# Kernel tuning notes

Measured on AMD Instinct MI355X. Metric: run time of the kernel, lower is better.

Reference implementation:

```python
import jax, jax.numpy as jnp
import numpy as np

B, N0, C, K, D = 16384, 1024, 12, 64, 3  # batch, feat dim, num_classes, num_clusters, ndim


def setup_inputs() -> dict:
    key = jax.random.key(0)
    ks = jax.random.split(key, 6)
    s = 0.02  # weight init scale
    return {
        "x": jax.random.normal(ks[0], (B, N0), dtype=jnp.float32),
        "Wfc": jax.random.normal(ks[1], (N0, C), dtype=jnp.float32) * s,
        "bfc": jnp.zeros((C,), dtype=jnp.float32),
        "Wbin": jax.random.normal(ks[2], (C, K, N0), dtype=jnp.float32) * s,
        "bbin": jnp.zeros((C, K), dtype=jnp.float32),
        "Wres": jax.random.normal(ks[3], (C, K, N0, D), dtype=jnp.float32) * s,
        "bres": jnp.zeros((C, K, D), dtype=jnp.float32),
        "centers": jax.random.normal(ks[4], (K, D), dtype=jnp.float32),
    }


def reference(x, Wfc, bfc, Wbin, bbin, Wres, bres, centers):
    # category head
    y0 = x @ Wfc + bfc                                            # [B, C]
    # per-class bin logits (batched over all classes at once)
    ybin = jnp.einsum("bn,ckn->bck", x, Wbin) + bbin              # [B, C, K]
    ind = jnp.argmax(ybin, axis=2)                                # [B, C] selected cluster per class
    # multires path: all (class, cluster) expert residuals, then one-hot select
    yres_all = jnp.einsum("bn,cknd->bckd", x, Wres) + bres        # [B, C, K, D]
    yres = jnp.take_along_axis(
        yres_all, ind[:, :, None, None], axis=2
    ).squeeze(2)                                                  # [B, C, D]
    # gather cluster centers and add residual
    y = centers[ind] + yres                                       # [B, C, D]
    # torch: stack over classes -> [C,B,D]; permute(1,2,0) -> [B, D, C]
    y1 = jnp.transpose(y, (0, 2, 1))                              # [B, D, C]
    return (y0, y1)
```

## Files before the change

### kernel.cpp

```cpp
#include <hip/hip_runtime.h>

typedef unsigned int uint32;
typedef unsigned long long uint64;
typedef unsigned short ushort16;
typedef __attribute__((ext_vector_type(8))) short bf16x8;
typedef __attribute__((ext_vector_type(4))) float f32x4;
typedef __attribute__((ext_vector_type(4))) uint32 u32x4;

#define B_SZ 16384
#define MARGIN 0.02f

__device__ __forceinline__ ushort16 f2bf(float f) {
  uint32 u = __float_as_uint(f);
  u += 0x7fffu + ((u >> 16) & 1u);
  return (ushort16)(u >> 16);
}
__device__ __forceinline__ float bf2f(ushort16 h) { return __uint_as_float(((uint32)h) << 16); }
__device__ __forceinline__ float bflo(uint32 u) { return __uint_as_float(u << 16); }
__device__ __forceinline__ float bfhi(uint32 u) { return __uint_as_float(u & 0xffff0000u); }
__device__ __forceinline__ uint32 pk2(float lo, float hi) {
  return ((uint32)f2bf(hi) << 16) | (uint32)f2bf(lo);
}
__device__ __forceinline__ int dot4(uint32 a, uint32 b, int c) {
#if __has_builtin(__builtin_amdgcn_sdot4)
  return __builtin_amdgcn_sdot4((int)a, (int)b, c, false);
#else
  int s = c;
#pragma unroll
  for (int k = 0; k < 4; ++k)
    s += (int)(char)(a >> (8 * k)) * (int)(char)(b >> (8 * k));
  return s;
#endif
}
__device__ __forceinline__ int q8(float v, float inv) {
  int q = (int)rintf(v * inv);
  return q > 127 ? 127 : (q < -127 ? -127 : q);
}

__global__ __launch_bounds__(256) void prep_all(
    const float* __restrict__ Wfc, const float* __restrict__ Wbin,
    const float* __restrict__ Wres, const float* __restrict__ x,
    ushort16* __restrict__ Wall, uint32* __restrict__ wq, float* __restrict__ swk,
    uint2* __restrict__ xb, uint32* __restrict__ xq, float* __restrict__ sxb) {
  __shared__ float red[256];
  const int blk = blockIdx.x;
  const int t = threadIdx.x;
  if (blk < 3584) {
    int idx = blk * 256 + t;
    int j = idx >> 10, n = idx & 1023;
    float v = 0.f;
    if (j < 12) v = Wfc[n * 12 + j];
    else if (j >= 64 && j < 832) v = Wbin[(size_t)(j - 64) * 1024 + n];
    Wall[idx] = f2bf(v);
  } else if (blk < 4352) {
    const int ck = blk - 3584;
    const float4* base4 = (const float4*)(Wres + (size_t)ck * 3072);
    float4 v0 = base4[3 * t], v1 = base4[3 * t + 1], v2 = base4[3 * t + 2];
    float vals[12] = {v0.x, v0.y, v0.z, v0.w, v1.x, v1.y, v1.z, v1.w, v2.x, v2.y, v2.z, v2.w};
    float m = 0.f;
#pragma unroll
    for (int i = 0; i < 12; ++i) m = fmaxf(m, fabsf(vals[i]));
    red[t] = m; __syncthreads();
    for (int s = 128; s; s >>= 1) { if (t < s) red[t] = fmaxf(red[t], red[t + s]); __syncthreads(); }
    float mx = fmaxf(red[0], 1e-20f);
    float inv = 127.f / mx;
    if (t == 0) swk[ck] = mx / 127.f;
#pragma unroll
    for (int d = 0; d < 3; ++d) {
      uint32 u = 0;
#pragma unroll
      for (int j = 0; j < 4; ++j)
        u |= ((uint32)(unsigned char)(char)q8(vals[j * 3 + d], inv)) << (8 * j);
      wq[((size_t)(ck * 3 + d) << 8) + t] = u;
    }
  } else {
    const int lane = t & 63;
    const int b = (blk - 4352) * 4 + (t >> 6);
    const float4* xr = (const float4*)(x + (size_t)b * 1024 + lane * 16);
    float4 v0 = xr[0], v1 = xr[1], v2 = xr[2], v3 = xr[3];
    float xv[16] = {v0.x, v0.y, v0.z, v0.w, v1.x, v1.y, v1.z, v1.w,
                    v2.x, v2.y, v2.z, v2.w, v3.x, v3.y, v3.z, v3.w};
    u32x4 pa, pb;
    pa.x = pk2(xv[0], xv[1]);  pa.y = pk2(xv[2], xv[3]);
    pa.z = pk2(xv[4], xv[5]);  pa.w = pk2(xv[6], xv[7]);
    pb.x = pk2(xv[8], xv[9]);  pb.y = pk2(xv[10], xv[11]);
    pb.z = pk2(xv[12], xv[13]); pb.w = pk2(xv[14], xv[15]);
    u32x4* xbrow = (u32x4*)((uint32*)xb + (size_t)b * 512);
    xbrow[2 * lane] = pa;
    xbrow[2 * lane + 1] = pb;
    float m = 0.f;
#pragma unroll
    for (int i = 0; i < 16; ++i) m = fmaxf(m, fabsf(xv[i]));
    for (int off = 32; off; off >>= 1) m = fmaxf(m, __shfl_xor(m, off));
    float mx = fmaxf(m, 1e-20f);
    float inv = 127.f / mx;
    if (lane == 0) sxb[b] = mx / 127.f;
    u32x4 qv;
#pragma unroll
    for (int q = 0; q < 4; ++q) {
      uint32 u = ((uint32)(unsigned char)(char)q8(xv[4 * q + 0], inv)) |
                 ((uint32)(unsigned char)(char)q8(xv[4 * q + 1], inv)) << 8 |
                 ((uint32)(unsigned char)(char)q8(xv[4 * q + 2], inv)) << 16 |
                 ((uint32)(unsigned char)(char)q8(xv[4 * q + 3], inv)) << 24;
      qv[q] = u;
    }
    ((u32x4*)(xq + (size_t)b * 256))[lane] = qv;
  }
}

__global__ void prep_wall_f(const float* __restrict__ Wfc, const float* __restrict__ Wbin,
                            ushort16* __restrict__ Wall) {
  int idx = blockIdx.x * 256 + threadIdx.x;
  int j = idx >> 10, n = idx & 1023;
  float v = 0.f;
  if (j < 12) v = Wfc[n * 12 + j];
  else if (j >= 64 && j < 832) v = Wbin[(size_t)(j - 64) * 1024 + n];
  Wall[idx] = f2bf(v);
}
__global__ void prep_wres(const float* __restrict__ Wres, ushort16* __restrict__ Wres_b) {
  int idx = blockIdx.x * 256 + threadIdx.x;
  int n = idx & 1023;
  int d = (idx >> 10) % 3;
  int ck = idx / 3072;
  Wres_b[idx] = f2bf(Wres[((size_t)ck * 1024 + n) * 3 + d]);
}

template<int XB>
__global__ __launch_bounds__(256) void gemm_mfma(
    const float* __restrict__ x, const ushort16* __restrict__ xb,
    const float* __restrict__ bfc, const float* __restrict__ bbin,
    const ushort16* __restrict__ Wall, ushort16* __restrict__ ybin,
    unsigned char* __restrict__ ind8, uint64* __restrict__ mask64,
    float* __restrict__ out) {
  __shared__ __align__(16) char smem[65536];
  const int t = threadIdx.x;
  const int lane = t & 63, wid = t >> 6;
  const int wm = wid & 1, wn = wid >> 1;

  int orig = blockIdx.x;
  int bid = (orig & 7) * 112 + (orig >> 3);
  int nb = bid % 7, mb = bid / 7;
  const int b0 = mb * 128;

  f32x4 acc[4][4];
#pragma unroll
  for (int i = 0; i < 4; ++i)
#pragma unroll
    for (int j = 0; j < 4; ++j) acc[i][j] = (f32x4){0.f, 0.f, 0.f, 0.f};

  const int lr = lane & 15, lq = lane >> 4;
  const int fxor = (lr & 7) << 4;
  const int gs = (lane & 7) ^ (lane >> 3);
  const int grw = lane >> 3;

#define GLDS(srcp, dstoff)                                                      \
  __builtin_amdgcn_global_load_lds(                                             \
      (const __attribute__((address_space(1))) uint32*)(srcp),                  \
      (__attribute__((address_space(3))) uint32*)(smem + (dstoff)), 16, 0, 0)

  if (XB) {
#pragma unroll
    for (int i = 0; i < 4; ++i) {
      int ch = i * 4 + wid, row = ch * 8 + grw;
      GLDS(xb + (size_t)(b0 + row) * 1024 + gs * 8, ch * 1024);
      GLDS(Wall + (size_t)(nb * 128 + row) * 1024 + gs * 8, 16384 + ch * 1024);
    }
    asm volatile("s_waitcnt vmcnt(0)" ::: "memory");
    __builtin_amdgcn_s_barrier();
    int cur = 0;
#pragma unroll 1
    for (int tt = 0; tt < 16; ++tt) {
      if (tt < 15) {
        int kc = (tt + 1) * 64;
        int nbase = (cur ^ 1) * 32768;
#pragma unroll
        for (int i = 0; i < 4; ++i) {
          int ch = i * 4 + wid, row = ch * 8 + grw;
          GLDS(xb + (size_t)(b0 + row) * 1024 + kc + gs * 8, nbase + ch * 1024);
          GLDS(Wall + (size_t)(nb * 128 + row) * 1024 + kc + gs * 8, nbase + 16384 + ch * 1024);
        }
      }
      asm volatile("" ::: "memory");
      const char* base = smem + cur * 32768;
#pragma unroll
      for (int kk = 0; kk < 2; ++kk) {
        int cbx = (kk * 64 + lq * 16) ^ fxor;
        bf16x8 af[4], bfr[4];
#pragma unroll
        for (int i = 0; i < 4; ++i)
          af[i] = *(const bf16x8*)(base + (wm * 64 + i * 16 + lr) * 128 + cbx);
#pragma unroll
        for (int j = 0; j < 4; ++j)
          bfr[j] = *(const bf16x8*)(base + 16384 + (wn * 64 + j * 16 + lr) * 128 + cbx);
#pragma unroll
        for (int i = 0; i < 4; ++i)
#pragma unroll
          for (int j = 0; j < 4; ++j)
            acc[i][j] = __builtin_amdgcn_mfma_f32_16x16x32_bf16(af[i], bfr[j], acc[i][j], 0, 0, 0);
      }
      if (tt < 15) {
        asm volatile("s_waitcnt vmcnt(0)" ::: "memory");
        __builtin_amdgcn_s_barrier();
        cur ^= 1;
      }
    }
  } else {
    for (int kc = 0; kc < 1024; kc += 64) {
      __syncthreads();
      const int sxor = ((t >> 3) & 7) << 4;
#pragma unroll
      for (int i = 0; i < 4; ++i) {
        int s = t + i * 256;
        int row = s >> 3, c8 = (s & 7) * 8;
        int dst = row * 128 + ((c8 * 2) ^ sxor);
        const float4* src = (const float4*)(x + (size_t)(b0 + row) * 1024 + kc + c8);
        float4 v0 = src[0], v1 = src[1];
        u32x4 pv;
        pv.x = pk2(v0.x, v0.y); pv.y = pk2(v0.z, v0.w);
        pv.z = pk2(v1.x, v1.y); pv.w = pk2(v1.z, v1.w);
        *(u32x4*)(smem + dst) = pv;
      }
#pragma unroll
      for (int i = 0; i < 4; ++i) {
        int s = t + i * 256;
        int row = s >> 3, c8 = (s & 7) * 8;
        int dst = 16384 + row * 128 + ((c8 * 2) ^ sxor);
        u32x4 v = *(const u32x4*)(Wall + (size_t)(nb * 128 + row) * 1024 + kc + c8);
        *(u32x4*)(smem + dst) = v;
      }
      __syncthreads();
#pragma unroll
      for (int kk = 0; kk < 2; ++kk) {
        int cbx = (kk * 64 + lq * 16) ^ fxor;
        bf16x8 af[4], bfr[4];
#pragma unroll
        for (int i = 0; i < 4; ++i)
          af[i] = *(const bf16x8*)(smem + (wm * 64 + i * 16 + lr) * 128 + cbx);
#pragma unroll
        for (int j = 0; j < 4; ++j)
          bfr[j] = *(const bf16x8*)(smem + 16384 + (wn * 64 + j * 16 + lr) * 128 + cbx);
#pragma unroll
        for (int i = 0; i < 4; ++i)
#pragma unroll
          for (int j = 0; j < 4; ++j)
            acc[i][j] = __builtin_amdgcn_mfma_f32_16x16x32_bf16(af[i], bfr[j], acc[i][j], 0, 0, 0);
      }
    }
  }
#undef GLDS

  const int g = 2 * nb + wn;
  if (g == 0) {
#pragma unroll
    for (int i = 0; i < 4; ++i)
#pragma unroll
      for (int r = 0; r < 4; ++r) {
        int gm = b0 + wm * 64 + i * 16 + lq * 4 + r;
        if (lr < 12) out[(size_t)gm * 12 + lr] = acc[i][0][r] + bfc[lr];
      }
    return;
  }
  if (g > 12) return;
  const int c = g - 1;
  if (XB == 0) {
#pragma unroll
    for (int i = 0; i < 4; ++i)
#pragma unroll
      for (int j = 0; j < 4; ++j)
#pragma unroll
        for (int r = 0; r < 4; ++r) {
          int gm = b0 + wm * 64 + i * 16 + lq * 4 + r;
          int col = j * 16 + lr;
          ybin[((size_t)gm * 12 + c) * 64 + col] = f2bf(acc[i][j][r] + bbin[c * 64 + col]);
        }
    return;
  }
  float bb[4];
#pragma unroll
  for (int j = 0; j < 4; ++j) bb[j] = bbin[c * 64 + j * 16 + lr];
#pragma unroll
  for (int i = 0; i < 4; ++i)
#pragma unroll
    for (int r = 0; r < 4; ++r) {
      float v0 = acc[i][0][r] + bb[0], v1 = acc[i][1][r] + bb[1];
      float v2 = acc[i][2][r] + bb[2], v3 = acc[i][3][r] + bb[3];
      float m1 = v0, m2 = -3.4e38f; int k1 = lr;
      if (v1 > m1) { m2 = m1; m1 = v1; k1 = 16 + lr; } else m2 = fmaxf(m2, v1);
      if (v2 > m1) { m2 = m1; m1 = v2; k1 = 32 + lr; } else m2 = fmaxf(m2, v2);
      if (v3 > m1) { m2 = m1; m1 = v3; k1 = 48 + lr; } else m2 = fmaxf(m2, v3);
#pragma unroll
      for (int off = 1; off < 16; off <<= 1) {
        float om1 = __shfl_xor(m1, off);
        int   ok1 = __shfl_xor(k1, off);
        float om2 = __shfl_xor(m2, off);
        bool take = (om1 > m1) || (om1 == m1 && ok1 < k1);
        float lose = take ? m1 : om1;
        m2 = fmaxf(fmaxf(m2, om2), lose);
        if (take) { m1 = om1; k1 = ok1; }
      }
      float thr = m1 - MARGIN;
      uint64 bl0 = __ballot(v0 >= thr);
      uint64 bl1 = __ballot(v1 >= thr);
      uint64 bl2 = __ballot(v2 >= thr);
      uint64 bl3 = __ballot(v3 >= thr);
      if (lr == 0) {
        int row = wm * 64 + i * 16 + lq * 4 + r;
        uint64 mk = ((bl0 >> (lq * 16)) & 0xffffull) |
                    (((bl1 >> (lq * 16)) & 0xffffull) << 16) |
                    (((bl2 >> (lq * 16)) & 0xffffull) << 32) |
                    (((bl3 >> (lq * 16)) & 0xffffull) << 48);
        int gp = (b0 + row) * 12 + c;
        ind8[gp] = (unsigned char)(k1 | ((m1 - m2 <= MARGIN) ? 128 : 0));
        mask64[gp] = mk;
      }
    }
}

__global__ __launch_bounds__(256) void compact_k(const unsigned char* __restrict__ ind8,
                                                 uint32* __restrict__ cnt,
                                                 uint32* __restrict__ wl) {
  const int b = blockIdx.x * 256 + threadIdx.x;
  const int lane = threadIdx.x & 63;
  const uint32* p = (const uint32*)(ind8 + b * 12);
  uint32 d0 = p[0], d1 = p[1], d2 = p[2];
  uint32 fmask = 0;
#pragma unroll
  for (int j = 0; j < 4; ++j) {
    if ((d0 >> (8 * j)) & 128u) fmask |= 1u << j;
    if ((d1 >> (8 * j)) & 128u) fmask |= 1u << (4 + j);
    if ((d2 >> (8 * j)) & 128u) fmask |= 1u << (8 + j);
  }
  uint64 bal = __ballot(fmask != 0);
  uint32 base = 0;
  if (lane == 0 && bal) base = atomicAdd(cnt, (uint32)__popcll(bal));
  base = __shfl(base, 0);
  if (fmask) {
    int rank = (int)__popcll(bal & ((1ull << lane) - 1ull));
    wl[base + rank] = (uint32)b | (fmask << 14);
  }
}

__global__ __launch_bounds__(256) void tail_k(
    const float* __restrict__ x, const float* __restrict__ Wbin,
    const float* __restrict__ bbin, const float* __restrict__ bres,
    const float* __restrict__ centers, const unsigned char* __restrict__ ind8,
    const uint64* __restrict__ mask64, const uint32* __restrict__ wq,
    const float* __restrict__ swk, const uint32* __restrict__ xq,
    const float* __restrict__ sxb, const uint32* __restrict__ cnt,
    const uint32* __restrict__ wl, float* __restrict__ out) {
  const int lane = threadIdx.x & 63;
  const int w = threadIdx.x >> 6;

  if (blockIdx.x < 4096) {
    const uint32 wv_id = blockIdx.x * 4 + w;
    if (wv_id >= *cnt) return;
    const uint32 e = wl[wv_id];
    const int b = (int)(e & 16383u);
    uint32 fmask = e >> 14;

    float xv[16];
    const float4* xr = (const float4*)(x + (size_t)b * 1024 + lane * 16);
#pragma unroll
    for (int q = 0; q < 4; ++q) {
      float4 vv = xr[q];
      xv[4 * q] = vv.x; xv[4 * q + 1] = vv.y; xv[4 * q + 2] = vv.z; xv[4 * q + 3] = vv.w;
    }
    const float sx = sxb[b];
    const float inv = (sx > 0.f) ? 1.f / sx : 0.f;
    uint32 xi[4];
#pragma unroll
    for (int q = 0; q < 4; ++q)
      xi[q] = ((uint32)(unsigned char)(char)q8(xv[4 * q + 0], inv)) |
              ((uint32)(unsigned char)(char)q8(xv[4 * q + 1], inv)) << 8 |
              ((uint32)(unsigned char)(char)q8(xv[4 * q + 2], inv)) << 16 |
              ((uint32)(unsigned char)(char)q8(xv[4 * q + 3], inv)) << 24;
    const size_t obase = (size_t)B_SZ * 12 + (size_t)b * 36;

#pragma unroll 1
    while (fmask) {
      const int c = __ffs(fmask) - 1;
      fmask &= fmask - 1;
      uint64 mask = mask64[b * 12 + c];
      double best = -1.0e300;
      int bk = 0;
#pragma unroll 1
      while (mask) {
        int kk[4];
        int nc = 0;
        while (mask && nc < 4) { kk[nc++] = __ffsll(mask) - 1; mask &= mask - 1; }
#pragma unroll
        for (int j = 1; j < 4; ++j) if (j >= nc) kk[j] = kk[0];
        double s[4] = {0.0, 0.0, 0.0, 0.0};
#pragma unroll
        for (int ci = 0; ci < 4; ++ci) {
          const float4* wr4 = (const float4*)(Wbin + ((size_t)c * 64 + kk[ci]) * 1024 + lane * 16);
#pragma unroll
          for (int q = 0; q < 4; ++q) {
            float4 wvv = wr4[q];
            s[ci] += (double)xv[4 * q] * (double)wvv.x + (double)xv[4 * q + 1] * (double)wvv.y +
                     (double)xv[4 * q + 2] * (double)wvv.z + (double)xv[4 * q + 3] * (double)wvv.w;
          }
        }
        for (int off = 32; off; off >>= 1) {
#pragma unroll
          for (int ci = 0; ci < 4; ++ci) s[ci] += __shfl_xor(s[ci], off);
        }
#pragma unroll
        for (int ci = 0; ci < 4; ++ci) {
          double sv = s[ci] + (double)bbin[c * 64 + kk[ci]];
          if (ci < nc && sv > best) { best = sv; bk = kk[ci]; }
        }
      }
      const int ck = c * 64 + bk;
      const uint32* wr = wq + (size_t)ck * 768;
      int acc[3];
#pragma unroll
      for (int d = 0; d < 3; ++d) {
        u32x4 wvq = *(const u32x4*)(wr + d * 256 + lane * 4);
        int ss = dot4(xi[0], wvq.x, 0);
        ss = dot4(xi[1], wvq.y, ss);
        ss = dot4(xi[2], wvq.z, ss);
        acc[d] = dot4(xi[3], wvq.w, ss);
      }
      for (int off = 32; off; off >>= 1) {
        acc[0] += __shfl_xor(acc[0], off);
        acc[1] += __shfl_xor(acc[1], off);
        acc[2] += __shfl_xor(acc[2], off);
      }
      if (lane == 0) {
        float sc = sx * swk[ck];
        out[obase + 0 * 12 + c] = centers[bk * 3 + 0] + bres[ck * 3 + 0] + sc * (float)acc[0];
        out[obase + 1 * 12 + c] = centers[bk * 3 + 1] + bres[ck * 3 + 1] + sc * (float)acc[1];
        out[obase + 2 * 12 + c] = centers[bk * 3 + 2] + bres[ck * 3 + 2] + sc * (float)acc[2];
      }
    }
    return;
  }

  const int b = blockIdx.x - 4096;

  const u32x4 xi = *(const u32x4*)(xq + (size_t)b * 256 + lane * 4);
  const float sx = sxb[b];
  const size_t obase = (size_t)B_SZ * 12 + (size_t)b * 36;

  int iv[3], ind[3], ck[3];
  u32x4 wv[3][3];
#pragma unroll
  for (int cc = 0; cc < 3; ++cc) {
    int c = w * 3 + cc;
    iv[cc] = ind8[b * 12 + c];
    ind[cc] = iv[cc] & 63;
    ck[cc] = c * 64 + ind[cc];
    const uint32* wr = wq + (size_t)ck[cc] * 768;
#pragma unroll
    for (int d = 0; d < 3; ++d)
      wv[cc][d] = *(const u32x4*)(wr + d * 256 + lane * 4);
  }
  int acc[3][3];
#pragma unroll
  for (int cc = 0; cc < 3; ++cc)
#pragma unroll
    for (int d = 0; d < 3; ++d) {
      int s = dot4(xi.x, wv[cc][d].x, 0);
      s = dot4(xi.y, wv[cc][d].y, s);
      s = dot4(xi.z, wv[cc][d].z, s);
      acc[cc][d] = dot4(xi.w, wv[cc][d].w, s);
    }
  for (int off = 32; off; off >>= 1) {
#pragma unroll
    for (int cc = 0; cc < 3; ++cc)
#pragma unroll
      for (int d = 0; d < 3; ++d)
        acc[cc][d] += __shfl_xor(acc[cc][d], off);
  }
  if (lane == 0) {
#pragma unroll
    for (int cc = 0; cc < 3; ++cc) {
      if (iv[cc] & 128) continue;
      int c = w * 3 + cc;
      float sc = sx * swk[ck[cc]];
      out[obase + 0 * 12 + c] = centers[ind[cc] * 3 + 0] + bres[ck[cc] * 3 + 0] + sc * (float)acc[cc][0];
      out[obase + 1 * 12 + c] = centers[ind[cc] * 3 + 1] + bres[ck[cc] * 3 + 1] + sc * (float)acc[cc][1];
      out[obase + 2 * 12 + c] = centers[ind[cc] * 3 + 2] + bres[ck[cc] * 3 + 2] + sc * (float)acc[cc][2];
    }
  }
}

__global__ __launch_bounds__(256) void select2(
    const float* __restrict__ x, const float* __restrict__ Wbin,
    const float* __restrict__ bbin, const float* __restrict__ bres,
    const float* __restrict__ centers, const ushort16* __restrict__ Wres_b,
    const ushort16* __restrict__ ybin, float* __restrict__ out) {
  const int lane = threadIdx.x & 63;
  const int w = threadIdx.x >> 6;
  const int b = blockIdx.x;
  float xv[16];
  {
    const float4* xr = (const float4*)(x + (size_t)b * 1024 + lane * 16);
#pragma unroll
    for (int q = 0; q < 4; ++q) {
      float4 v = xr[q];
      xv[4 * q] = v.x; xv[4 * q + 1] = v.y; xv[4 * q + 2] = v.z; xv[4 * q + 3] = v.w;
    }
  }
  const size_t obase = (size_t)B_SZ * 12 + (size_t)b * 36;
#pragma unroll 1
  for (int cc = 0; cc < 3; ++cc) {
    const int c = w * 3 + cc;
    float v = bf2f(ybin[((size_t)b * 12 + c) * 64 + lane]);
    float m1 = v, m2 = -3.4e38f;
    int k1 = lane;
    for (int off = 32; off; off >>= 1) {
      float om1 = __shfl_xor(m1, off);
      int   ok1 = __shfl_xor(k1, off);
      float om2 = __shfl_xor(m2, off);
      bool take = (om1 > m1) || (om1 == m1 && ok1 < k1);
      float lose = take ? m1 : om1;
      m2 = fmaxf(fmaxf(m2, om2), lose);
      if (take) { m1 = om1; k1 = ok1; }
    }
    int ind = k1;
    if (m1 - m2 <= MARGIN) {
      unsigned long long mask = __ballot(v >= m1 - MARGIN);
      double best = -1.0e300;
      int bk = 0;
      while (mask) {
        int k = __ffsll(mask) - 1;
        mask &= (mask - 1);
        const float4* wr4 = (const float4*)(Wbin + ((size_t)c * 64 + k) * 1024 + lane * 16);
        double s = 0.0;
#pragma unroll
        for (int q = 0; q < 4; ++q) {
          float4 wv = wr4[q];
          s += (double)xv[4 * q] * (double)wv.x + (double)xv[4 * q + 1] * (double)wv.y +
               (double)xv[4 * q + 2] * (double)wv.z + (double)xv[4 * q + 3] * (double)wv.w;
        }
        for (int off = 32; off; off >>= 1) s += __shfl_xor(s, off);
        s += (double)bbin[c * 64 + k];
        if (s > best) { best = s; bk = k; }
      }
      ind = bk;
    }
    const ushort16* wr = Wres_b + ((size_t)(c * 64 + ind) * 3) * 1024;
    float a[3] = {0.f, 0.f, 0.f};
#pragma unroll
    for (int d = 0; d < 3; ++d) {
      const u32x4* pp = (const u32x4*)(wr + d * 1024 + lane * 16);
      u32x4 w0 = pp[0], w1 = pp[1];
      uint32 uw[8] = {w0.x, w0.y, w0.z, w0.w, w1.x, w1.y, w1.z, w1.w};
#pragma unroll
      for (int q = 0; q < 8; ++q) {
        a[d] = fmaf(xv[2 * q],     bflo(uw[q]), a[d]);
        a[d] = fmaf(xv[2 * q + 1], bfhi(uw[q]), a[d]);
      }
    }
    for (int off = 32; off; off >>= 1) {
      a[0] += __shfl_xor(a[0], off);
      a[1] += __shfl_xor(a[1], off);
      a[2] += __shfl_xor(a[2], off);
    }
    if (lane == 0) {
      int ck = c * 64 + ind;
      out[obase + 0 * 12 + c] = centers[ind * 3 + 0] + bres[ck * 3 + 0] + a[0];
      out[obase + 1 * 12 + c] = centers[ind * 3 + 1] + bres[ck * 3 + 1] + a[1];
      out[obase + 2 * 12 + c] = centers[ind * 3 + 2] + bres[ck * 3 + 2] + a[2];
    }
  }
}

extern "C" void kernel_launch(void* const* d_in, const int* in_sizes, int n_in,
                              void* d_out, int out_size, void* d_ws, size_t ws_size,
                              hipStream_t stream) {
  const float* x       = (const float*)d_in[0];
  const float* Wfc     = (const float*)d_in[1];
  const float* bfc     = (const float*)d_in[2];
  const float* Wbin    = (const float*)d_in[3];
  const float* bbin    = (const float*)d_in[4];
  const float* Wres    = (const float*)d_in[5];
  const float* bres    = (const float*)d_in[6];
  const float* centers = (const float*)d_in[7];
  float* out = (float*)d_out;

  char* ws = (char*)d_ws;
  ushort16* Wall = (ushort16*)ws;
  if (ws_size >= 56430592ull) {
    uint32*        wq     = (uint32*)(ws + 1835008);
    float*         swk    = (float*)(ws + 4194304);
    unsigned char* ind8   = (unsigned char*)(ws + 4197376);
    uint64*        mask64 = (uint64*)(ws + 4393984);
    ushort16*      xb     = (ushort16*)(ws + 5966848);
    uint32*        xq     = (uint32*)(ws + 39521280);
    float*         sxb    = (float*)(ws + 56298496);
    uint32*        cnt    = (uint32*)(ws + 56364032);
    uint32*        wl     = (uint32*)(ws + 56364288);

    hipMemsetAsync(cnt, 0, 4, stream);
    prep_all<<<8448, 256, 0, stream>>>(Wfc, Wbin, Wres, x, Wall, wq, swk,
                                       (uint2*)xb, xq, sxb);
    gemm_mfma<1><<<896, 256, 0, stream>>>(x, xb, bfc, bbin, Wall,
                                          (ushort16*)nullptr, ind8, mask64, out);
    compact_k<<<64, 256, 0, stream>>>(ind8, cnt, wl);
    tail_k<<<20480, 256, 0, stream>>>(x, Wbin, bbin, bres, centers, ind8, mask64,
                                      wq, swk, xq, sxb, cnt, wl, out);
  } else {
    ushort16* Wres_b = (ushort16*)(ws + 1835008);
    ushort16* ybin   = (ushort16*)(ws + 6553600);
    prep_wall_f<<<3584, 256, 0, stream>>>(Wfc, Wbin, Wall);
    prep_wres<<<9216, 256, 0, stream>>>(Wres, Wres_b);
    gemm_mfma<0><<<896, 256, 0, stream>>>(x, (const ushort16*)ws, bfc, bbin, Wall,
                                          ybin, (unsigned char*)nullptr,
                                          (uint64*)nullptr, out);
    select2<<<B_SZ, 256, 0, stream>>>(x, Wbin, bbin, bres, centers, Wres_b, ybin, out);
  }
}
```

Before: 159.5 us.

## Deepen GEMM LDS pipeline to four-stage ring of half-K tiles

Replaces the double-buffered 64-wide K tiles in the bf16 MFMA path with a 4-slot ring of 32-wide K tiles, keeping three stages of async global-to-LDS loads in flight and using partial vmcnt waits. The aim is to hide global load latency better and avoid draining all outstanding loads each iteration. In exchange it needs twice as many barriers per K, a changed swizzle for 64-byte rows, and more careful vmcnt accounting. A read of a ring slot that a later stage overwrites would be a correctness risk.

```diff
diff --git a/kernel.cpp b/kernel.cpp
--- a/kernel.cpp
+++ b/kernel.cpp
@@ -149,9 +149,6 @@
     for (int j = 0; j < 4; ++j) acc[i][j] = (f32x4){0.f, 0.f, 0.f, 0.f};
 
   const int lr = lane & 15, lq = lane >> 4;
-  const int fxor = (lr & 7) << 4;
-  const int gs = (lane & 7) ^ (lane >> 3);
-  const int grw = lane >> 3;
 
 #define GLDS(srcp, dstoff)                                                      \
   __builtin_amdgcn_global_load_lds(                                             \
@@ -159,52 +156,52 @@
       (__attribute__((address_space(3))) uint32*)(smem + (dstoff)), 16, 0, 0)
 
   if (XB) {
-#pragma unroll
-    for (int i = 0; i < 4; ++i) {
-      int ch = i * 4 + wid, row = ch * 8 + grw;
-      GLDS(xb + (size_t)(b0 + row) * 1024 + gs * 8, ch * 1024);
-      GLDS(Wall + (size_t)(nb * 128 + row) * 1024 + gs * 8, 16384 + ch * 1024);
-    }
-    asm volatile("s_waitcnt vmcnt(0)" ::: "memory");
-    __builtin_amdgcn_s_barrier();
-    int cur = 0;
+    const int gs2 = (lane & 3) ^ ((lane >> 2) & 3);
+    const int grw2 = lane >> 2;
+    const int ch0 = wid * 2, ch1 = wid * 2 + 1;
+    const ushort16* arow0 = xb + (size_t)(b0 + ch0 * 16 + grw2) * 1024 + gs2 * 8;
+    const ushort16* arow1 = xb + (size_t)(b0 + ch1 * 16 + grw2) * 1024 + gs2 * 8;
+    const ushort16* brow0 = Wall + (size_t)(nb * 128 + ch0 * 16 + grw2) * 1024 + gs2 * 8;
+    const ushort16* brow1 = Wall + (size_t)(nb * 128 + ch1 * 16 + grw2) * 1024 + gs2 * 8;
+
+#define STAGE_HALF(h)                                                           \
+    {                                                                           \
+      int bb_ = ((h) & 3) * 16384;                                              \
+      int kc_ = (h) * 32;                                                       \
+      GLDS(arow0 + kc_, bb_ + ch0 * 1024);                                      \
+      GLDS(arow1 + kc_, bb_ + ch1 * 1024);                                      \
+      GLDS(brow0 + kc_, bb_ + 8192 + ch0 * 1024);                               \
+      GLDS(brow1 + kc_, bb_ + 8192 + ch1 * 1024);                               \
+    }
+
+    STAGE_HALF(0); STAGE_HALF(1); STAGE_HALF(2);
+    const int cbx2 = (lq * 16) ^ ((lr & 3) << 4);
+    const int arow_off = (wm * 64 + lr) * 64;
+    const int brow_off = (wn * 64 + lr) * 64;
 #pragma unroll 1
-    for (int tt = 0; tt < 16; ++tt) {
-      if (tt < 15) {
-        int kc = (tt + 1) * 64;
-        int nbase = (cur ^ 1) * 32768;
-#pragma unroll
-        for (int i = 0; i < 4; ++i) {
-          int ch = i * 4 + wid, row = ch * 8 + grw;
-          GLDS(xb + (size_t)(b0 + row) * 1024 + kc + gs * 8, nbase + ch * 1024);
-          GLDS(Wall + (size_t)(nb * 128 + row) * 1024 + kc + gs * 8, nbase + 16384 + ch * 1024);
-        }
-      }
-      asm volatile("" ::: "memory");
-      const char* base = smem + cur * 32768;
-#pragma unroll
-      for (int kk = 0; kk < 2; ++kk) {
-        int cbx = (kk * 64 + lq * 16) ^ fxor;
-        bf16x8 af[4], bfr[4];
-#pragma unroll
-        for (int i = 0; i < 4; ++i)
-          af[i] = *(const bf16x8*)(base + (wm * 64 + i * 16 + lr) * 128 + cbx);
+    for (int h = 0; h < 32; ++h) {
+      if (h < 30)      asm volatile("s_waitcnt vmcnt(8)" ::: "memory");
+      else if (h == 30) asm volatile("s_waitcnt vmcnt(4)" ::: "memory");
+      else              asm volatile("s_waitcnt vmcnt(0)" ::: "memory");
+      __builtin_amdgcn_s_barrier();
+      if (h < 29) STAGE_HALF(h + 3);
+      const char* base = smem + (h & 3) * 16384;
+      bf16x8 af[4], bfr[4];
+#pragma unroll
+      for (int i = 0; i < 4; ++i)
+        af[i] = *(const bf16x8*)(base + arow_off + i * 1024 + cbx2);
+#pragma unroll
+      for (int j = 0; j < 4; ++j)
+        bfr[j] = *(const bf16x8*)(base + 8192 + brow_off + j * 1024 + cbx2);
+#pragma unroll
+      for (int i = 0; i < 4; ++i)
 #pragma unroll
         for (int j = 0; j < 4; ++j)
-          bfr[j] = *(const bf16x8*)(base + 16384 + (wn * 64 + j * 16 + lr) * 128 + cbx);
-#pragma unroll
-        for (int i = 0; i < 4; ++i)
-#pragma unroll
-          for (int j = 0; j < 4; ++j)
-            acc[i][j] = __builtin_amdgcn_mfma_f32_16x16x32_bf16(af[i], bfr[j], acc[i][j], 0, 0, 0);
-      }
-      if (tt < 15) {
-        asm volatile("s_waitcnt vmcnt(0)" ::: "memory");
-        __builtin_amdgcn_s_barrier();
-        cur ^= 1;
-      }
-    }
+          acc[i][j] = __builtin_amdgcn_mfma_f32_16x16x32_bf16(af[i], bfr[j], acc[i][j], 0, 0, 0);
+    }
+#undef STAGE_HALF
   } else {
+    const int fxor = (lr & 7) << 4;
     for (int kc = 0; kc < 1024; kc += 64) {
       __syncthreads();
       const int sxor = ((t >> 3) & 7) << 4;
```

After: 158.6 us. Within noise of the previous version (-0.6%).
